# Kernel optimization log

Hardware: AMD Instinct MI355X
Metric: run time of the kernel (lower is better)

Reference implementation:

```python
import jax, jax.numpy as jnp
import numpy as np

DELTA_V = 0.5
DELTA_D = 3.0
ALPHA = 1.0
BETA = 1.0
GAMMA = 0.001
K = 5  # max instance label (labels 1..K; 0 = background)


def setup_inputs() -> dict:
    key = jax.random.key(0)
    k1, k2 = jax.random.split(key)
    B, D, H, W = 8, 8, 512, 1024
    embedding = jax.random.normal(k1, (B, D, H, W), dtype=jnp.float32)
    instance_mask = jax.random.randint(k2, (B, H, W), 0, K + 1, dtype=jnp.int32)
    return {"embedding": embedding, "instance_mask": instance_mask}


def _disc_loss(embedding, instance_mask):
    B, D, H, W = embedding.shape
    P = H * W
    emb = embedding.transpose(0, 2, 3, 1).reshape(B, P, D)      # [B,P,D]
    labels = instance_mask.reshape(B, P)                         # [B,P]

    # one-hot over instance labels 1..K (background excluded)
    onehot = (labels[..., None] == jnp.arange(1, K + 1, dtype=labels.dtype)).astype(emb.dtype)  # [B,P,K]
    counts = onehot.sum(axis=1)                                  # [B,K]
    present = counts > 0                                         # [B,K]
    presentf = present.astype(emb.dtype)
    N = presentf.sum(axis=-1)                                    # [B] num instances

    # per-instance centers via segment mean
    sums = jnp.einsum('bpd,bpk->bkd', emb, onehot)               # [B,K,D]
    centers = sums / jnp.maximum(counts, 1.0)[..., None]         # [B,K,D]

    # ---- variance loss: per-pixel distance to own center ----
    idx = jnp.clip(labels - 1, 0, K - 1)                         # [B,P]
    c_pix = jnp.take_along_axis(centers, idx[..., None], axis=1) # [B,P,D]
    d = jnp.sqrt(jnp.sum((emb - c_pix) ** 2, axis=-1))           # [B,P]
    val = jnp.maximum(d - DELTA_V, 0.0) ** 2                     # [B,P]
    inst_sum = jnp.einsum('bp,bpk->bk', val, onehot)             # [B,K]
    inst_mean = inst_sum / jnp.maximum(counts, 1.0)
    loss_var_b = (inst_mean * presentf).sum(-1) / jnp.maximum(N, 1.0)  # [B]

    # ---- distance loss: pairwise center hinge ----
    diff = centers[:, :, None, :] - centers[:, None, :, :]       # [B,K,K,D]
    dist_sq = jnp.sum(diff ** 2, axis=-1)                        # [B,K,K]
    iu = jnp.triu(jnp.ones((K, K), dtype=bool), k=1)             # i<j
    pair_mask = present[:, :, None] & present[:, None, :] & iu   # [B,K,K]
    safe_dist = jnp.sqrt(jnp.where(pair_mask, dist_sq, 1.0))
    term = jnp.maximum(2.0 * DELTA_D - safe_dist, 0.0) ** 2 * pair_mask.astype(emb.dtype)
    n_pairs = N * (N - 1.0) / 2.0
    loss_dist_b = term.sum((-1, -2)) / jnp.where(N > 1, n_pairs, 1.0)  # [B]

    # ---- regularization: mean norm of present centers ----
    c_norm = jnp.sqrt(jnp.where(present, jnp.sum(centers ** 2, axis=-1), 1.0))
    loss_reg_b = (c_norm * presentf).sum(-1) / jnp.maximum(N, 1.0)     # [B]

    # ---- batch mean over images that have at least one instance ----
    has = (N > 0).astype(emb.dtype)                              # [B]
    denom = jnp.maximum(has.sum(), 1.0)
    loss_var = (loss_var_b * has).sum() / denom
    loss_dist = (loss_dist_b * has).sum() / denom
    loss_reg = (loss_reg_b * has).sum() / denom
    total = ALPHA * loss_var + BETA * loss_dist + GAMMA * loss_reg
    return (total, loss_var, loss_dist, loss_reg)


def reference(embedding, instance_mask):
    return _disc_loss(embedding, instance_mask)
```

## Files before the change

kernel.cpp:

```cpp
#include <hip/hip_runtime.h>
#include <math.h>

constexpr int NB = 8, ND = 8, NP = 512 * 1024, NG = NP / 4, NK = 5;
constexpr int BPB  = 128;
constexpr int NBLK = NB * BPB;
constexpr int GPB  = NG / BPB;
constexpr int ITER = GPB / 256;
constexpr int PSTR = 48;

constexpr float DELTA_V = 0.5f, TWO_DELTA_D = 6.0f, GAMMA = 0.001f;
#define SCOPE __HIP_MEMORY_SCOPE_AGENT

constexpr int OFF_TOT = 64, OFF_VP = 512, OFF_P1 = 16384;

__device__ __forceinline__ float wave_sum(float v) {
#pragma unroll
    for (int off = 32; off > 0; off >>= 1) v += __shfl_down(v, off, 64);
    return v;
}

__global__ __launch_bounds__(256) void k1_partials(
    const float* __restrict__ emb, const int* __restrict__ mask,
    float* __restrict__ ws)
{
    const int b   = blockIdx.x / BPB;
    const int blk = blockIdx.x % BPB;
    const float4* emb4 = (const float4*)emb + (size_t)b * ND * NG;
    const int4*   m4   = (const int4*)mask + (size_t)b * NG;
    const int base = blk * GPB;

    float acc[NK][ND], cnt[NK];
#pragma unroll
    for (int k = 0; k < NK; ++k) {
        cnt[k] = 0.f;
#pragma unroll
        for (int d = 0; d < ND; ++d) acc[k][d] = 0.f;
    }

#pragma unroll 1
    for (int i = 0; i < ITER; ++i) {
        const int g = base + i * 256 + threadIdx.x;
        const int4 m = m4[g];
        float4 e[ND];
#pragma unroll
        for (int d = 0; d < ND; ++d) e[d] = emb4[(size_t)d * NG + g];
        const int labs[4] = {m.x, m.y, m.z, m.w};
#pragma unroll
        for (int j = 0; j < 4; ++j) {
            const int lab = labs[j];
#pragma unroll
            for (int k = 0; k < NK; ++k) {
                const bool sel = (lab == k + 1);
                cnt[k] += sel ? 1.f : 0.f;
#pragma unroll
                for (int d = 0; d < ND; ++d)
                    acc[k][d] += sel ? ((const float*)&e[d])[j] : 0.f;
            }
        }
    }

    __shared__ float part[4][PSTR];
    const int lane = threadIdx.x & 63, wave = threadIdx.x >> 6;
#pragma unroll
    for (int k = 0; k < NK; ++k) {
#pragma unroll
        for (int d = 0; d < ND; ++d) {
            const float r = wave_sum(acc[k][d]);
            if (lane == 0) part[wave][k * ND + d] = r;
        }
        const float rc = wave_sum(cnt[k]);
        if (lane == 0) part[wave][NK * ND + k] = rc;
    }
    __syncthreads();
    if (threadIdx.x < 45) {
        const float s = part[0][threadIdx.x] + part[1][threadIdx.x] +
                        part[2][threadIdx.x] + part[3][threadIdx.x];
        ws[OFF_P1 + (size_t)threadIdx.x * NBLK + blockIdx.x] = s;
    }
    if (blockIdx.x == 0 && threadIdx.x == 0)
        ((int*)ws)[0] = 0;
}

__global__ __launch_bounds__(256) void k2_hinge(
    const float* __restrict__ emb, const int* __restrict__ mask,
    float* __restrict__ ws, float* __restrict__ out)
{
    const int b   = blockIdx.x / BPB;
    const int blk = blockIdx.x % BPB;

    __shared__ float red1[45][4];
    __shared__ float csh[PSTR];
    __shared__ float cLDS[6][ND];
    __shared__ float part[4][8];
    __shared__ float vred[NB][NK][4];
    __shared__ float tsh[NB][PSTR];
    __shared__ bool  amlast;

    if (threadIdx.x < 180) {
        const int v = threadIdx.x >> 2, q = threadIdx.x & 3;
        const float* p = ws + OFF_P1 + (size_t)v * NBLK + b * BPB + q * 32;
        float s = 0.f;
#pragma unroll
        for (int i = 0; i < 32; ++i) s += p[i];
        red1[v][q] = s;
    }
    __syncthreads();
    if (threadIdx.x < 45) {
        const float s = red1[threadIdx.x][0] + red1[threadIdx.x][1] +
                        red1[threadIdx.x][2] + red1[threadIdx.x][3];
        csh[threadIdx.x] = s;
        if (blk == 0)
            __hip_atomic_store(&ws[OFF_TOT + b * PSTR + threadIdx.x], s,
                               __ATOMIC_RELEASE, SCOPE);
    }
    __syncthreads();
    if (threadIdx.x < 48) {
        const int row = threadIdx.x >> 3, d = threadIdx.x & 7;
        float v = 0.f;
        if (row > 0)
            v = csh[(row - 1) * ND + d] / fmaxf(csh[NK * ND + (row - 1)], 1.f);
        cLDS[row][d] = v;
    }
    __syncthreads();

    const float4* emb4 = (const float4*)emb + (size_t)b * ND * NG;
    const int4*   m4   = (const int4*)mask + (size_t)b * NG;
    const int base = blk * GPB;

    float vacc[NK] = {0.f, 0.f, 0.f, 0.f, 0.f};
#pragma unroll 1
    for (int i = 0; i < ITER; ++i) {
        const int g = base + i * 256 + threadIdx.x;
        const int4 m = m4[g];
        float4 e[ND];
#pragma unroll
        for (int d = 0; d < ND; ++d) e[d] = emb4[(size_t)d * NG + g];
        const int labs[4] = {m.x, m.y, m.z, m.w};
#pragma unroll
        for (int j = 0; j < 4; ++j) {
            const int lab = labs[j];
            const float4* crow = (const float4*)&cLDS[lab][0];
            const float4 c0 = crow[0], c1 = crow[1];
            const float cd[8] = {c0.x, c0.y, c0.z, c0.w, c1.x, c1.y, c1.z, c1.w};
            float dsq = 0.f;
#pragma unroll
            for (int d = 0; d < ND; ++d) {
                const float diff = ((const float*)&e[d])[j] - cd[d];
                dsq = fmaf(diff, diff, dsq);
            }
            const float hv = fmaxf(sqrtf(dsq) - DELTA_V, 0.f);
            const float val = hv * hv;
#pragma unroll
            for (int k = 0; k < NK; ++k)
                vacc[k] += (lab == k + 1) ? val : 0.f;
        }
    }

    const int lane = threadIdx.x & 63, wave = threadIdx.x >> 6;
#pragma unroll
    for (int k = 0; k < NK; ++k) {
        const float r = wave_sum(vacc[k]);
        if (lane == 0) part[wave][k] = r;
    }
    __syncthreads();
    if (threadIdx.x < NK) {
        const float s = part[0][threadIdx.x] + part[1][threadIdx.x] +
                        part[2][threadIdx.x] + part[3][threadIdx.x];
        __hip_atomic_store(&ws[OFF_VP + (size_t)blockIdx.x * 8 + threadIdx.x], s,
                           __ATOMIC_RELEASE, SCOPE);
    }
    __syncthreads();
    if (threadIdx.x == 0) {
        const int old = __hip_atomic_fetch_add((int*)ws, 1, __ATOMIC_ACQ_REL, SCOPE);
        amlast = (old == NBLK - 1);
    }
    __syncthreads();
    if (!amlast) return;

    if (threadIdx.x < 160) {
        const int bb = threadIdx.x / 20, r = threadIdx.x % 20;
        const int k = r >> 2, q = r & 3;
        float s = 0.f;
#pragma unroll
        for (int i = 0; i < 32; ++i)
            s += __hip_atomic_load(&ws[OFF_VP + (size_t)(bb * BPB + q * 32 + i) * 8 + k],
                                   __ATOMIC_RELAXED, SCOPE);
        vred[bb][k][q] = s;
    }
    for (int t = threadIdx.x; t < NB * PSTR; t += 256) {
        const int bb = t / PSTR, j = t % PSTR;
        tsh[bb][j] = __hip_atomic_load(&ws[OFF_TOT + bb * PSTR + j],
                                       __ATOMIC_RELAXED, SCOPE);
    }
    __syncthreads();
    if (threadIdx.x == 0) {
        float tv = 0.f, td = 0.f, tr = 0.f, hs = 0.f;
        for (int bb = 0; bb < NB; ++bb) {
            float cc[NK], CC[NK][ND];
            bool pres[NK];
            float N = 0.f;
            for (int k = 0; k < NK; ++k) {
                cc[k] = tsh[bb][NK * ND + k];
                pres[k] = cc[k] > 0.f;
                if (pres[k]) N += 1.f;
                const float inv = 1.f / fmaxf(cc[k], 1.f);
                for (int d = 0; d < ND; ++d)
                    CC[k][d] = tsh[bb][k * ND + d] * inv;
            }
            float lv = 0.f;
            for (int k = 0; k < NK; ++k)
                if (pres[k]) {
                    const float vs = vred[bb][k][0] + vred[bb][k][1] +
                                     vred[bb][k][2] + vred[bb][k][3];
                    lv += vs / fmaxf(cc[k], 1.f);
                }
            lv /= fmaxf(N, 1.f);

            float ld = 0.f;
            for (int i2 = 0; i2 < NK; ++i2)
                for (int j2 = i2 + 1; j2 < NK; ++j2)
                    if (pres[i2] && pres[j2]) {
                        float dsq = 0.f;
                        for (int d = 0; d < ND; ++d) {
                            const float df = CC[i2][d] - CC[j2][d];
                            dsq = fmaf(df, df, dsq);
                        }
                        const float t = fmaxf(TWO_DELTA_D - sqrtf(dsq), 0.f);
                        ld += t * t;
                    }
            const float npairs = N * (N - 1.f) * 0.5f;
            ld /= (N > 1.f) ? npairs : 1.f;

            float lr = 0.f;
            for (int k = 0; k < NK; ++k)
                if (pres[k]) {
                    float sq = 0.f;
                    for (int d = 0; d < ND; ++d) sq = fmaf(CC[k][d], CC[k][d], sq);
                    lr += sqrtf(sq);
                }
            lr /= fmaxf(N, 1.f);

            if (N > 0.f) { tv += lv; td += ld; tr += lr; hs += 1.f; }
        }
        const float den = fmaxf(hs, 1.f);
        tv /= den; td /= den; tr /= den;
        out[0] = tv + td + GAMMA * tr;
        out[1] = tv;
        out[2] = td;
        out[3] = tr;
    }
}

extern "C" void kernel_launch(void* const* d_in, const int* in_sizes, int n_in,
                              void* d_out, int out_size, void* d_ws, size_t ws_size,
                              hipStream_t stream) {
    const float* emb  = (const float*)d_in[0];
    const int*   mask = (const int*)d_in[1];
    float* ws = (float*)d_ws;
    k1_partials<<<dim3(NBLK), dim3(256), 0, stream>>>(emb, mask, ws);
    k2_hinge<<<dim3(NBLK), dim3(256), 0, stream>>>(emb, mask, ws, (float*)d_out);
}
```

Before: 292.0 us.

## Double blocks per image and fully unroll two-group loads per thread

Raises blocks per image from 128 to 256, so each thread handles exactly two pixel groups. Both groups' embedding and mask loads are issued up front instead of running a serial loop, which puts more loads in flight per thread. A waves-per-EU hint is added to both kernels, and the workspace offsets and final reduction strides are scaled to match the larger block count. The cost is higher register pressure from holding 16 float4 values live, plus more partials in the cross-block reduction.

After: 369.8 us. 26.6% more time.

```diff
diff --git a/kernel.cpp b/kernel.cpp
--- a/kernel.cpp
+++ b/kernel.cpp
@@ -2,16 +2,15 @@
 #include <math.h>
 
 constexpr int NB = 8, ND = 8, NP = 512 * 1024, NG = NP / 4, NK = 5;
-constexpr int BPB  = 128;
+constexpr int BPB  = 256;
 constexpr int NBLK = NB * BPB;
 constexpr int GPB  = NG / BPB;
-constexpr int ITER = GPB / 256;
 constexpr int PSTR = 48;
 
 constexpr float DELTA_V = 0.5f, TWO_DELTA_D = 6.0f, GAMMA = 0.001f;
 #define SCOPE __HIP_MEMORY_SCOPE_AGENT
 
-constexpr int OFF_TOT = 64, OFF_VP = 512, OFF_P1 = 16384;
+constexpr int OFF_TOT = 64, OFF_VP = 1024, OFF_P1 = 32768;
 
 __device__ __forceinline__ float wave_sum(float v) {
 #pragma unroll
@@ -19,15 +18,24 @@
     return v;
 }
 
-__global__ __launch_bounds__(256) void k1_partials(
-    const float* __restrict__ emb, const int* __restrict__ mask,
-    float* __restrict__ ws)
+__global__ __attribute__((amdgpu_waves_per_eu(2, 4))) __launch_bounds__(256)
+void k1_partials(const float* __restrict__ emb, const int* __restrict__ mask,
+                 float* __restrict__ ws)
 {
     const int b   = blockIdx.x / BPB;
     const int blk = blockIdx.x % BPB;
     const float4* emb4 = (const float4*)emb + (size_t)b * ND * NG;
     const int4*   m4   = (const int4*)mask + (size_t)b * NG;
-    const int base = blk * GPB;
+    const int g0 = blk * GPB + threadIdx.x;
+    const int g1 = g0 + 256;
+
+    const int4 m_a = m4[g0];
+    const int4 m_b = m4[g1];
+    float4 e_a[ND], e_b[ND];
+#pragma unroll
+    for (int d = 0; d < ND; ++d) e_a[d] = emb4[(size_t)d * NG + g0];
+#pragma unroll
+    for (int d = 0; d < ND; ++d) e_b[d] = emb4[(size_t)d * NG + g1];
 
     float acc[NK][ND], cnt[NK];
 #pragma unroll
@@ -37,14 +45,8 @@
         for (int d = 0; d < ND; ++d) acc[k][d] = 0.f;
     }
 
-#pragma unroll 1
-    for (int i = 0; i < ITER; ++i) {
-        const int g = base + i * 256 + threadIdx.x;
-        const int4 m = m4[g];
-        float4 e[ND];
-#pragma unroll
-        for (int d = 0; d < ND; ++d) e[d] = emb4[(size_t)d * NG + g];
-        const int labs[4] = {m.x, m.y, m.z, m.w};
+    {
+        const int labs[4] = {m_a.x, m_a.y, m_a.z, m_a.w};
 #pragma unroll
         for (int j = 0; j < 4; ++j) {
             const int lab = labs[j];
@@ -54,7 +56,22 @@
                 cnt[k] += sel ? 1.f : 0.f;
 #pragma unroll
                 for (int d = 0; d < ND; ++d)
-                    acc[k][d] += sel ? ((const float*)&e[d])[j] : 0.f;
+                    acc[k][d] += sel ? ((const float*)&e_a[d])[j] : 0.f;
+            }
+        }
+    }
+    {
+        const int labs[4] = {m_b.x, m_b.y, m_b.z, m_b.w};
+#pragma unroll
+        for (int j = 0; j < 4; ++j) {
+            const int lab = labs[j];
+#pragma unroll
+            for (int k = 0; k < NK; ++k) {
+                const bool sel = (lab == k + 1);
+                cnt[k] += sel ? 1.f : 0.f;
+#pragma unroll
+                for (int d = 0; d < ND; ++d)
+                    acc[k][d] += sel ? ((const float*)&e_b[d])[j] : 0.f;
             }
         }
     }
@@ -81,9 +98,9 @@
         ((int*)ws)[0] = 0;
 }
 
-__global__ __launch_bounds__(256) void k2_hinge(
-    const float* __restrict__ emb, const int* __restrict__ mask,
-    float* __restrict__ ws, float* __restrict__ out)
+__global__ __attribute__((amdgpu_waves_per_eu(2, 4))) __launch_bounds__(256)
+void k2_hinge(const float* __restrict__ emb, const int* __restrict__ mask,
+              float* __restrict__ ws, float* __restrict__ out)
 {
     const int b   = blockIdx.x / BPB;
     const int blk = blockIdx.x % BPB;
@@ -98,10 +115,10 @@
 
     if (threadIdx.x < 180) {
         const int v = threadIdx.x >> 2, q = threadIdx.x & 3;
-        const float* p = ws + OFF_P1 + (size_t)v * NBLK + b * BPB + q * 32;
+        const float* p = ws + OFF_P1 + (size_t)v * NBLK + b * BPB + q * 64;
         float s = 0.f;
 #pragma unroll
-        for (int i = 0; i < 32; ++i) s += p[i];
+        for (int i = 0; i < 64; ++i) s += p[i];
         red1[v][q] = s;
     }
     __syncthreads();
@@ -125,17 +142,20 @@
 
     const float4* emb4 = (const float4*)emb + (size_t)b * ND * NG;
     const int4*   m4   = (const int4*)mask + (size_t)b * NG;
-    const int base = blk * GPB;
+    const int g0 = blk * GPB + threadIdx.x;
+    const int g1 = g0 + 256;
+
+    const int4 m_a = m4[g0];
+    const int4 m_b = m4[g1];
+    float4 e_a[ND], e_b[ND];
+#pragma unroll
+    for (int d = 0; d < ND; ++d) e_a[d] = emb4[(size_t)d * NG + g0];
+#pragma unroll
+    for (int d = 0; d < ND; ++d) e_b[d] = emb4[(size_t)d * NG + g1];
 
     float vacc[NK] = {0.f, 0.f, 0.f, 0.f, 0.f};
-#pragma unroll 1
-    for (int i = 0; i < ITER; ++i) {
-        const int g = base + i * 256 + threadIdx.x;
-        const int4 m = m4[g];
-        float4 e[ND];
-#pragma unroll
-        for (int d = 0; d < ND; ++d) e[d] = emb4[(size_t)d * NG + g];
-        const int labs[4] = {m.x, m.y, m.z, m.w};
+    {
+        const int labs[4] = {m_a.x, m_a.y, m_a.z, m_a.w};
 #pragma unroll
         for (int j = 0; j < 4; ++j) {
             const int lab = labs[j];
@@ -145,7 +165,28 @@
             float dsq = 0.f;
 #pragma unroll
             for (int d = 0; d < ND; ++d) {
-                const float diff = ((const float*)&e[d])[j] - cd[d];
+                const float diff = ((const float*)&e_a[d])[j] - cd[d];
+                dsq = fmaf(diff, diff, dsq);
+            }
+            const float hv = fmaxf(sqrtf(dsq) - DELTA_V, 0.f);
+            const float val = hv * hv;
+#pragma unroll
+            for (int k = 0; k < NK; ++k)
+                vacc[k] += (lab == k + 1) ? val : 0.f;
+        }
+    }
+    {
+        const int labs[4] = {m_b.x, m_b.y, m_b.z, m_b.w};
+#pragma unroll
+        for (int j = 0; j < 4; ++j) {
+            const int lab = labs[j];
+            const float4* crow = (const float4*)&cLDS[lab][0];
+            const float4 c0 = crow[0], c1 = crow[1];
+            const float cd[8] = {c0.x, c0.y, c0.z, c0.w, c1.x, c1.y, c1.z, c1.w};
+            float dsq = 0.f;
+#pragma unroll
+            for (int d = 0; d < ND; ++d) {
+                const float diff = ((const float*)&e_b[d])[j] - cd[d];
                 dsq = fmaf(diff, diff, dsq);
             }
             const float hv = fmaxf(sqrtf(dsq) - DELTA_V, 0.f);
@@ -182,8 +223,8 @@
         const int k = r >> 2, q = r & 3;
         float s = 0.f;
 #pragma unroll
-        for (int i = 0; i < 32; ++i)
-            s += __hip_atomic_load(&ws[OFF_VP + (size_t)(bb * BPB + q * 32 + i) * 8 + k],
+        for (int i = 0; i < 64; ++i)
+            s += __hip_atomic_load(&ws[OFF_VP + (size_t)(bb * BPB + q * 64 + i) * 8 + k],
                                    __ATOMIC_RELAXED, SCOPE);
         vred[bb][k][q] = s;
     }
```

## Prefetch next tile in both passes and compute centers once per batch

Applied to the files above, without the earlier changes.

Both streaming loops now software-pipeline their global loads, fetching the next iteration's mask and embedding vectors while the current ones are processed, and the loops are fully unrolled. The per-batch center reduction moves out of every k2 block and into the last-arriving k1 block per image, found with a per-batch atomic counter. That block writes the centers to the workspace, so k2 blocks only read 48 floats instead of re-reducing 45x128 partials. A tiny init kernel zeroes the counters. The trade is more registers for the prefetch buffers, which may lower occupancy, plus one extra launch.

After: 395.3 us. +35.4%, slower.

```diff
diff --git a/kernel.cpp b/kernel.cpp
--- a/kernel.cpp
+++ b/kernel.cpp
@@ -11,23 +11,27 @@
 constexpr float DELTA_V = 0.5f, TWO_DELTA_D = 6.0f, GAMMA = 0.001f;
 #define SCOPE __HIP_MEMORY_SCOPE_AGENT
 
-constexpr int OFF_TOT = 64, OFF_VP = 512, OFF_P1 = 16384;
+constexpr int OFF_CEN = 64, OFF_TOT = 1024, OFF_VP = 2048, OFF_P1 = 16384;
 
 __device__ __forceinline__ float wave_sum(float v) {
 #pragma unroll
     for (int off = 32; off > 0; off >>= 1) v += __shfl_down(v, off, 64);
     return v;
+}
+
+__global__ void k0_init(int* wsi) {
+    if (threadIdx.x < 64) wsi[threadIdx.x] = 0;
 }
 
 __global__ __launch_bounds__(256) void k1_partials(
     const float* __restrict__ emb, const int* __restrict__ mask,
     float* __restrict__ ws)
 {
+    int* const wsi = (int*)ws;
     const int b   = blockIdx.x / BPB;
     const int blk = blockIdx.x % BPB;
     const float4* emb4 = (const float4*)emb + (size_t)b * ND * NG;
     const int4*   m4   = (const int4*)mask + (size_t)b * NG;
-    const int base = blk * GPB;
 
     float acc[NK][ND], cnt[NK];
 #pragma unroll
@@ -37,14 +41,23 @@
         for (int d = 0; d < ND; ++d) acc[k][d] = 0.f;
     }
 
-#pragma unroll 1
+    int g = blk * GPB + threadIdx.x;
+    int4 mc = m4[g];
+    float4 ec[ND];
+#pragma unroll
+    for (int d = 0; d < ND; ++d) ec[d] = emb4[(size_t)d * NG + g];
+
+#pragma unroll
     for (int i = 0; i < ITER; ++i) {
-        const int g = base + i * 256 + threadIdx.x;
-        const int4 m = m4[g];
-        float4 e[ND];
-#pragma unroll
-        for (int d = 0; d < ND; ++d) e[d] = emb4[(size_t)d * NG + g];
-        const int labs[4] = {m.x, m.y, m.z, m.w};
+        int4 mn;
+        float4 en[ND];
+        if (i + 1 < ITER) {
+            const int gn = g + 256;
+            mn = m4[gn];
+#pragma unroll
+            for (int d = 0; d < ND; ++d) en[d] = emb4[(size_t)d * NG + gn];
+        }
+        const int labs[4] = {mc.x, mc.y, mc.z, mc.w};
 #pragma unroll
         for (int j = 0; j < 4; ++j) {
             const int lab = labs[j];
@@ -54,8 +67,14 @@
                 cnt[k] += sel ? 1.f : 0.f;
 #pragma unroll
                 for (int d = 0; d < ND; ++d)
-                    acc[k][d] += sel ? ((const float*)&e[d])[j] : 0.f;
+                    acc[k][d] += sel ? ((const float*)&ec[d])[j] : 0.f;
             }
+        }
+        if (i + 1 < ITER) {
+            mc = mn;
+#pragma unroll
+            for (int d = 0; d < ND; ++d) ec[d] = en[d];
+            g += 256;
         }
     }
 
@@ -75,33 +94,28 @@
     if (threadIdx.x < 45) {
         const float s = part[0][threadIdx.x] + part[1][threadIdx.x] +
                         part[2][threadIdx.x] + part[3][threadIdx.x];
-        ws[OFF_P1 + (size_t)threadIdx.x * NBLK + blockIdx.x] = s;
-    }
-    if (blockIdx.x == 0 && threadIdx.x == 0)
-        ((int*)ws)[0] = 0;
-}
-
-__global__ __launch_bounds__(256) void k2_hinge(
-    const float* __restrict__ emb, const int* __restrict__ mask,
-    float* __restrict__ ws, float* __restrict__ out)
-{
-    const int b   = blockIdx.x / BPB;
-    const int blk = blockIdx.x % BPB;
+        __hip_atomic_store(&ws[OFF_P1 + (size_t)threadIdx.x * NBLK + blockIdx.x],
+                           s, __ATOMIC_RELEASE, SCOPE);
+    }
+    __syncthreads();
+
+    __shared__ bool amlast;
+    if (threadIdx.x == 0) {
+        const int old = __hip_atomic_fetch_add(&wsi[8 + b], 1, __ATOMIC_ACQ_REL, SCOPE);
+        amlast = (old == BPB - 1);
+    }
+    __syncthreads();
+    if (!amlast) return;
 
     __shared__ float red1[45][4];
     __shared__ float csh[PSTR];
-    __shared__ float cLDS[6][ND];
-    __shared__ float part[4][8];
-    __shared__ float vred[NB][NK][4];
-    __shared__ float tsh[NB][PSTR];
-    __shared__ bool  amlast;
-
     if (threadIdx.x < 180) {
         const int v = threadIdx.x >> 2, q = threadIdx.x & 3;
         const float* p = ws + OFF_P1 + (size_t)v * NBLK + b * BPB + q * 32;
         float s = 0.f;
 #pragma unroll
-        for (int i = 0; i < 32; ++i) s += p[i];
+        for (int i = 0; i < 32; ++i)
+            s += __hip_atomic_load(&p[i], __ATOMIC_RELAXED, SCOPE);
         red1[v][q] = s;
     }
     __syncthreads();
@@ -109,9 +123,7 @@
         const float s = red1[threadIdx.x][0] + red1[threadIdx.x][1] +
                         red1[threadIdx.x][2] + red1[threadIdx.x][3];
         csh[threadIdx.x] = s;
-        if (blk == 0)
-            __hip_atomic_store(&ws[OFF_TOT + b * PSTR + threadIdx.x], s,
-                               __ATOMIC_RELEASE, SCOPE);
+        ws[OFF_TOT + b * PSTR + threadIdx.x] = s;
     }
     __syncthreads();
     if (threadIdx.x < 48) {
@@ -119,23 +131,48 @@
         float v = 0.f;
         if (row > 0)
             v = csh[(row - 1) * ND + d] / fmaxf(csh[NK * ND + (row - 1)], 1.f);
-        cLDS[row][d] = v;
-    }
+        ws[OFF_CEN + b * 64 + threadIdx.x] = v;
+    }
+}
+
+__global__ __launch_bounds__(256) void k2_hinge(
+    const float* __restrict__ emb, const int* __restrict__ mask,
+    float* __restrict__ ws, float* __restrict__ out)
+{
+    int* const wsi = (int*)ws;
+    const int b   = blockIdx.x / BPB;
+    const int blk = blockIdx.x % BPB;
+
+    __shared__ float cLDS[6][ND];
+    __shared__ float part[4][8];
+    __shared__ bool  amlast;
+
+    if (threadIdx.x < 48)
+        cLDS[threadIdx.x >> 3][threadIdx.x & 7] = ws[OFF_CEN + b * 64 + threadIdx.x];
     __syncthreads();
 
     const float4* emb4 = (const float4*)emb + (size_t)b * ND * NG;
     const int4*   m4   = (const int4*)mask + (size_t)b * NG;
-    const int base = blk * GPB;
 
     float vacc[NK] = {0.f, 0.f, 0.f, 0.f, 0.f};
-#pragma unroll 1
+
+    int g = blk * GPB + threadIdx.x;
+    int4 mc = m4[g];
+    float4 ec[ND];
+#pragma unroll
+    for (int d = 0; d < ND; ++d) ec[d] = emb4[(size_t)d * NG + g];
+
+#pragma unroll
     for (int i = 0; i < ITER; ++i) {
-        const int g = base + i * 256 + threadIdx.x;
-        const int4 m = m4[g];
-        float4 e[ND];
-#pragma unroll
-        for (int d = 0; d < ND; ++d) e[d] = emb4[(size_t)d * NG + g];
-        const int labs[4] = {m.x, m.y, m.z, m.w};
+        int4 mn;
+        float4 en[ND];
+        if (i + 1 < ITER) {
+            const int gn = g + 256;
+            mn = m4[gn];
+#pragma unroll
+            for (int d = 0; d < ND; ++d) en[d] = emb4[(size_t)d * NG + gn];
+        }
+        const int labs[4] = {mc.x, mc.y, mc.z, mc.w};
 #pragma unroll
         for (int j = 0; j < 4; ++j) {
             const int lab = labs[j];
@@ -145,7 +182,7 @@
             float dsq = 0.f;
 #pragma unroll
             for (int d = 0; d < ND; ++d) {
-                const float diff = ((const float*)&e[d])[j] - cd[d];
+                const float diff = ((const float*)&ec[d])[j] - cd[d];
                 dsq = fmaf(diff, diff, dsq);
             }
             const float hv = fmaxf(sqrtf(dsq) - DELTA_V, 0.f);
@@ -153,6 +190,12 @@
 #pragma unroll
             for (int k = 0; k < NK; ++k)
                 vacc[k] += (lab == k + 1) ? val : 0.f;
+        }
+        if (i + 1 < ITER) {
+            mc = mn;
+#pragma unroll
+            for (int d = 0; d < ND; ++d) ec[d] = en[d];
+            g += 256;
         }
     }
 
@@ -171,12 +214,14 @@
     }
     __syncthreads();
     if (threadIdx.x == 0) {
-        const int old = __hip_atomic_fetch_add((int*)ws, 1, __ATOMIC_ACQ_REL, SCOPE);
+        const int old = __hip_atomic_fetch_add(&wsi[0], 1, __ATOMIC_ACQ_REL, SCOPE);
         amlast = (old == NBLK - 1);
     }
     __syncthreads();
     if (!amlast) return;
 
+    __shared__ float vred[NB][NK][4];
+    __shared__ float tsh[NB][PSTR];
     if (threadIdx.x < 160) {
         const int bb = threadIdx.x / 20, r = threadIdx.x % 20;
         const int k = r >> 2, q = r & 3;
@@ -189,8 +234,7 @@
     }
     for (int t = threadIdx.x; t < NB * PSTR; t += 256) {
         const int bb = t / PSTR, j = t % PSTR;
-        tsh[bb][j] = __hip_atomic_load(&ws[OFF_TOT + bb * PSTR + j],
-                                       __ATOMIC_RELAXED, SCOPE);
+        tsh[bb][j] = ws[OFF_TOT + bb * PSTR + j];
     }
     __syncthreads();
     if (threadIdx.x == 0) {
@@ -257,6 +301,7 @@
     const float* emb  = (const float*)d_in[0];
     const int*   mask = (const int*)d_in[1];
     float* ws = (float*)d_ws;
+    k0_init<<<dim3(1), dim3(64), 0, stream>>>((int*)ws);
     k1_partials<<<dim3(NBLK), dim3(256), 0, stream>>>(emb, mask, ws);
     k2_hinge<<<dim3(NBLK), dim3(256), 0, stream>>>(emb, mask, ws, (float*)d_out);
 }
```
